# Kernel tuning notes

Measured on AMD Instinct MI355X. Metric: run time of the kernel, lower is better.

The kernel has to match this reference:

```python
import jax, jax.numpy as jnp
import numpy as np
from jax import lax

N_LAYERS = 10
N_BLOCKS = 3
N_STACK = N_LAYERS * N_BLOCKS  # 30
WIDTH = 512
SKIP_W = 256
CH = 1
QUANT = 256
BOTTLENECK = 16
KSIZE = 3
SCALE = 2 ** (N_LAYERS - 1)  # 512, nearest upsample factor
B, T = 1, 16384
T_EMB = T // SCALE  # 32


def causal_conv(x, w, b, dilation):
    # x: [B,Cin,T], w: [Cout,Cin,K] -> causal dilated conv, output [B,Cout,T]
    k = w.shape[-1]
    pad = (k - 1) * dilation
    y = lax.conv_general_dilated(x, w, window_strides=(1,), padding=[(pad, 0)],
                                 rhs_dilation=(dilation,),
                                 dimension_numbers=('NCH', 'OIH', 'NCH'))
    return y + b[None, :, None]


def conv1x1(x, w, b):
    # x: [B,Cin,T], w: [Cout,Cin]
    return jnp.einsum('oc,bct->bot', w, x) + b[None, :, None]


def setup_inputs() -> dict:
    key = jax.random.key(0)
    ks = jax.random.split(key, 24)
    s = 0.05
    inp = {
        'x': jax.random.normal(ks[0], (B, CH, T), jnp.float32),
        'embedding': jax.random.normal(ks[1], (B, BOTTLENECK, T_EMB), jnp.float32),
        'w_init': jax.random.normal(ks[2], (WIDTH, CH, KSIZE), jnp.float32) * s,
        'b_init': jnp.zeros((WIDTH,), jnp.float32),
        'w_iskip': jax.random.normal(ks[3], (SKIP_W, WIDTH), jnp.float32) * s,
        'b_iskip': jnp.zeros((SKIP_W,), jnp.float32),
        'w_dil': jax.random.normal(ks[4], (N_STACK, 2 * WIDTH, WIDTH, KSIZE), jnp.float32) * s,
        'b_dil': jnp.zeros((N_STACK, 2 * WIDTH), jnp.float32),
        'w_cond': jax.random.normal(ks[5], (N_STACK, 2 * WIDTH, BOTTLENECK), jnp.float32) * s,
        'b_cond': jnp.zeros((N_STACK, 2 * WIDTH), jnp.float32),
        'w_res': jax.random.normal(ks[6], (N_STACK, WIDTH, WIDTH), jnp.float32) * s,
        'b_res': jnp.zeros((N_STACK, WIDTH), jnp.float32),
        'w_skip': jax.random.normal(ks[7], (N_STACK, SKIP_W, WIDTH), jnp.float32) * s,
        'b_skip': jnp.zeros((N_STACK, SKIP_W), jnp.float32),
        'w_fskip': jax.random.normal(ks[8], (SKIP_W, SKIP_W), jnp.float32) * s,
        'b_fskip': jnp.zeros((SKIP_W,), jnp.float32),
        'w_fcond': jax.random.normal(ks[9], (SKIP_W, BOTTLENECK), jnp.float32) * s,
        'b_fcond': jnp.zeros((SKIP_W,), jnp.float32),
        'w_quant': jax.random.normal(ks[10], (QUANT, SKIP_W), jnp.float32) * s,
        'b_quant': jnp.zeros((QUANT,), jnp.float32),
    }
    return inp


def reference(x, embedding, w_init, b_init, w_iskip, b_iskip, w_dil, b_dil,
              w_cond, b_cond, w_res, b_res, w_skip, b_skip,
              w_fskip, b_fskip, w_fcond, b_fcond, w_quant, b_quant):
    # initial causal conv (kernel 3, dilation 1) + initial skip 1x1
    h = causal_conv(x, w_init, b_init, 1)            # [B,WIDTH,T]
    skip = conv1x1(h, w_iskip, b_iskip)              # [B,SKIP_W,T]
    for i in range(N_STACK):
        dilation = 2 ** (i % N_LAYERS)
        cond = conv1x1(embedding, w_cond[i], b_cond[i])      # [B,2W,T_EMB]
        cond_up = jnp.repeat(cond, SCALE, axis=-1)           # nearest upsample -> [B,2W,T]
        dilated = causal_conv(h, w_dil[i], b_dil[i], dilation) + cond_up
        filters = jax.nn.sigmoid(dilated[:, :WIDTH, :])
        gates = jnp.tanh(dilated[:, WIDTH:, :])
        pre = filters * gates
        h = h + conv1x1(pre, w_res[i], b_res[i])
        skip = skip + conv1x1(pre, w_skip[i], b_skip[i])
    skip = conv1x1(jax.nn.relu(skip), w_fskip, b_fskip)
    fcond = jnp.repeat(conv1x1(embedding, w_fcond, b_fcond), SCALE, axis=-1)
    skip = skip + fcond
    return conv1x1(jax.nn.relu(skip), w_quant, b_quant)     # [B,QUANT,T]
```

## Files before the change

kernel.cpp:

```cpp
#include <hip/hip_runtime.h>


typedef _Float16 f16x8 __attribute__((ext_vector_type(8)));
typedef float f32x4 __attribute__((ext_vector_type(4)));

#define NSTACK 30
#define TLEN   16384

typedef __attribute__((address_space(1))) const unsigned int glob_u32;
typedef __attribute__((address_space(3))) unsigned int lds_u32;

__device__ __forceinline__ void gll16(const unsigned short* g, unsigned short* l) {
  __builtin_amdgcn_global_load_lds((glob_u32*)g, (lds_u32*)l, 16, 0, 0);
}

__device__ __forceinline__ unsigned short f2h(float x) {
  union { _Float16 h; unsigned short u; } c;
  c.h = (_Float16)x;
  return c.u;
}
__device__ __forceinline__ unsigned pack2(float a, float b) {
  return (unsigned)f2h(a) | ((unsigned)f2h(b) << 16);
}
__device__ __forceinline__ float uplo(unsigned u){ union{unsigned v;_Float16 h[2];}c; c.v=u; return (float)c.h[0]; }
__device__ __forceinline__ float uphi(unsigned u){ union{unsigned v;_Float16 h[2];}c; c.v=u; return (float)c.h[1]; }
__device__ __forceinline__ f16x8 ldh(const unsigned short* p) {
  return *(const f16x8*)p;
}
__device__ __forceinline__ float sigmoidf_(float x){ return 1.0f/(1.0f+__expf(-x)); }
__device__ __forceinline__ float tanhf_(float x){ return 1.0f - 2.0f/(__expf(2.0f*x)+1.0f); }
#define MFMA16(a,b,c) __builtin_amdgcn_mfma_f32_16x16x32_f16((a),(b),(c),0,0,0)


__global__ void cast_f16_kernel(const float* __restrict__ src,
                                unsigned short* __restrict__ dst, int n4) {
  int g = blockIdx.x*256 + threadIdx.x;
  if (g >= n4) return;
  f32x4 v = *(const f32x4*)(src + 4*(size_t)g);
  unsigned int* d = (unsigned int*)(dst + 4*(size_t)g);
  d[0] = pack2(v[0], v[1]);
  d[1] = pack2(v[2], v[3]);
}

__global__ void transpose_wdil_kernel(const float* __restrict__ src,
                                      unsigned short* __restrict__ dst) {
  int g = blockIdx.x*256 + threadIdx.x;
  if (g >= NSTACK*1024*512) return;
  int c = g & 511;
  int m = (g >> 9) & 1023;
  int i = g >> 19;
  const float* s = src + (size_t)g*3;
  #pragma unroll
  for (int tap=0; tap<3; ++tap)
    dst[(((size_t)i*3+tap)*1024 + m)*512 + c] = f2h(s[tap]);
}

__global__ void cond_kernel(const float* __restrict__ emb,
                            const float* __restrict__ w_cond, const float* __restrict__ b_cond,
                            const float* __restrict__ b_dil,
                            const float* __restrict__ w_fcond, const float* __restrict__ b_fcond,
                            float* __restrict__ cond_all, float* __restrict__ fcond_all) {
  int g = blockIdx.x*256 + threadIdx.x;
  if (g < NSTACK*1024) {
    float acc[32];
    float base = b_cond[g] + b_dil[g];
    #pragma unroll
    for (int e=0;e<32;++e) acc[e] = base;
    #pragma unroll
    for (int c=0;c<16;++c) {
      float wv = w_cond[(size_t)g*16 + c];
      #pragma unroll
      for (int e=0;e<32;++e) acc[e] += wv * emb[c*32+e];
    }
    #pragma unroll
    for (int e=0;e<32;++e) cond_all[(size_t)g*32+e] = acc[e];
  } else if (g < NSTACK*1024 + 256) {
    int m = g - NSTACK*1024;
    float acc[32];
    float base = b_fcond[m];
    #pragma unroll
    for (int e=0;e<32;++e) acc[e] = base;
    #pragma unroll
    for (int c=0;c<16;++c) {
      float wv = w_fcond[(size_t)m*16 + c];
      #pragma unroll
      for (int e=0;e<32;++e) acc[e] += wv * emb[c*32+e];
    }
    #pragma unroll
    for (int e=0;e<32;++e) fcond_all[(size_t)m*32+e] = acc[e];
  }
}

__global__ void h0_kernel(const float* __restrict__ x, const float* __restrict__ w_init,
                          const float* __restrict__ b_init,
                          unsigned short* __restrict__ h_h16) {
  int g = blockIdx.x*256 + threadIdx.x;
  int t = g >> 7;
  int c = (g & 127) << 2;
  float xm2 = (t>=2)? x[t-2] : 0.f;
  float xm1 = (t>=1)? x[t-1] : 0.f;
  float x0  = x[t];
  float hv[4];
  #pragma unroll
  for (int r=0;r<4;++r) {
    int cc = c + r;
    hv[r] = w_init[cc*3+0]*xm2 + w_init[cc*3+1]*xm1 + w_init[cc*3+2]*x0 + b_init[cc];
  }
  unsigned int* hb = (unsigned int*)&h_h16[(size_t)t*512 + c];
  hb[0] = pack2(hv[0],hv[1]); hb[1] = pack2(hv[2],hv[3]);
}

__global__ __launch_bounds__(512) void skip_init_kernel(
    const unsigned short* __restrict__ h_h16, const unsigned short* __restrict__ Wiskip,
    const float* __restrict__ b_iskip, unsigned short* __restrict__ skip16) {
  int tid=threadIdx.x, w=tid>>6, l=tid&63, lr=l&15, lc=l>>4;
  int tb = blockIdx.x<<6;
  f32x4 acc[2][4];
  #pragma unroll
  for (int mf=0;mf<2;++mf)
    #pragma unroll
    for (int nf=0;nf<4;++nf) acc[mf][nf] = {0.f,0.f,0.f,0.f};
  for (int kc=0;kc<512;kc+=32) {
    f16x8 b[4];
    #pragma unroll
    for (int nf=0;nf<4;++nf)
      b[nf] = ldh(&h_h16[(size_t)(tb+16*nf+lr)*512 + kc + lc*8]);
    #pragma unroll
    for (int mf=0;mf<2;++mf) {
      f16x8 a = ldh(&Wiskip[(size_t)(w*32+16*mf+lr)*512 + kc + lc*8]);
      #pragma unroll
      for (int nf=0;nf<4;++nf)
        acc[mf][nf] = MFMA16(a, b[nf], acc[mf][nf]);
    }
  }
  #pragma unroll
  for (int mf=0;mf<2;++mf)
    #pragma unroll
    for (int nf=0;nf<4;++nf) {
      int s0 = w*32+16*mf+4*lc;
      int t  = tb+16*nf+lr;
      unsigned int* pp = (unsigned int*)&skip16[(size_t)t*256+s0];
      pp[0] = pack2(acc[mf][nf][0]+b_iskip[s0+0], acc[mf][nf][1]+b_iskip[s0+1]);
      pp[1] = pack2(acc[mf][nf][2]+b_iskip[s0+2], acc[mf][nf][3]+b_iskip[s0+3]);
    }
}

__global__ __launch_bounds__(256, 4) void dil_kernel(
    const unsigned short* __restrict__ h_in,
    unsigned short* __restrict__ pre,
    const unsigned short* __restrict__ A_dil,
    const float* __restrict__ cond,
    const unsigned short* __restrict__ zerobuf,
    int dilation) {
  __shared__ unsigned short Ab[2][128][32];
  __shared__ unsigned short Bb[2][128][32];
  const int tid = threadIdx.x;
  const int w = tid >> 6, l = tid & 63;
  const int lr = l & 15, lc = l >> 4;
  const int nt = blockIdx.x & 127, mt = blockIdx.x >> 7;
  const int tb = nt << 7;
  const int e  = tb >> 9;
  const int wr = w >> 1, wc = w & 1;

  const int srowA0 = (w<<5) + (l>>2);
  const int schunk = (l & 3) << 3;

  f32x4 fa[2][4], ga[2][4];
  #pragma unroll
  for (int mf=0;mf<2;++mf)
    #pragma unroll
    for (int nf=0;nf<4;++nf) { fa[mf][nf] = {0.f,0.f,0.f,0.f}; ga[mf][nf] = {0.f,0.f,0.f,0.f}; }

  auto stage = [&](int buf, int s){
    const int tap = s >> 4;
    const int kc  = (s & 15) << 5;
    const int shift = (2 - tap) * dilation;
    const unsigned short* Abase = A_dil + (size_t)tap * (1024*512) + kc + schunk;
    #pragma unroll
    for (int j=0;j<2;++j){
      const int r = srowA0 + (j<<4);
      const int m = mt*64 + r + ((r>>6)*448);
      gll16(Abase + (size_t)m*512, &Ab[buf][(w<<5)+(j<<4)][0]);
      const int t = tb + r - shift;
      const unsigned short* srcB = (t >= 0) ? (h_in + (size_t)t*512 + kc + schunk)
                                            : (zerobuf + schunk);
      gll16(srcB, &Bb[buf][(w<<5)+(j<<4)][0]);
    }
  };

  stage(0, 0);
  for (int s=0; s<48; ++s) {
    const int cur = s & 1;
    __syncthreads();
    if (s+1 < 48) stage(cur^1, s+1);
    f16x8 af[2], ag[2], bf[4];
    #pragma unroll
    for (int mf=0;mf<2;++mf){
      const int row = (wr<<5) + (mf<<4) + lr;
      af[mf] = ldh(&Ab[cur][row][lc<<3]);
      ag[mf] = ldh(&Ab[cur][64+row][lc<<3]);
    }
    #pragma unroll
    for (int nf=0;nf<4;++nf)
      bf[nf] = ldh(&Bb[cur][(wc<<6)+(nf<<4)+lr][lc<<3]);
    #pragma unroll
    for (int mf=0;mf<2;++mf)
      #pragma unroll
      for (int nf=0;nf<4;++nf){
        fa[mf][nf] = MFMA16(af[mf], bf[nf], fa[mf][nf]);
        ga[mf][nf] = MFMA16(ag[mf], bf[nf], ga[mf][nf]);
      }
  }

  #pragma unroll
  for (int mf=0;mf<2;++mf)
    #pragma unroll
    for (int nf=0;nf<4;++nf){
      const int m0 = mt*64 + (wr<<5) + (mf<<4) + (lc<<2);
      const int t  = tb + (wc<<6) + (nf<<4) + lr;
      float pv[4];
      #pragma unroll
      for (int r=0;r<4;++r){
        float f = fa[mf][nf][r] + cond[(size_t)(m0+r)*32 + e];
        float g = ga[mf][nf][r] + cond[(size_t)(m0+r+512)*32 + e];
        pv[r] = sigmoidf_(f) * tanhf_(g);
      }
      unsigned int* pp = (unsigned int*)&pre[(size_t)t*512 + m0];
      pp[0] = pack2(pv[0], pv[1]);
      pp[1] = pack2(pv[2], pv[3]);
    }
}

__global__ __launch_bounds__(256, 3) void ressk_kernel(
    const unsigned short* __restrict__ pre,
    const unsigned short* __restrict__ h_in,
    unsigned short* __restrict__ h_out,
    unsigned short* __restrict__ skip16,
    const unsigned short* __restrict__ Wres,
    const unsigned short* __restrict__ Wskip,
    const float* __restrict__ b_res,
    const float* __restrict__ b_skip) {
  __shared__ unsigned short Ab[2][128][32];
  __shared__ unsigned short Bb[2][128][32];
  const int tid = threadIdx.x;
  const int w = tid >> 6, l = tid & 63;
  const int lr = l & 15, lc = l >> 4;
  const int nt = blockIdx.x & 127, mt = blockIdx.x >> 7;
  const int tb = nt << 7;
  const int wr = w >> 1, wc = w & 1;
  const bool isres = (mt < 4);
  const unsigned short* W = isres ? Wres : Wskip;
  const int mrow0 = (isres ? mt : (mt-4)) * 128;

  const int srowA0 = (w<<5) + (l>>2);
  const int schunk = (l & 3) << 3;

  f32x4 acc[4][4];
  #pragma unroll
  for (int mf=0;mf<4;++mf)
    #pragma unroll
    for (int nf=0;nf<4;++nf) acc[mf][nf] = {0.f,0.f,0.f,0.f};

  auto stage = [&](int buf, int s){
    const int kc = s << 5;
    #pragma unroll
    for (int j=0;j<2;++j){
      const int r = srowA0 + (j<<4);
      gll16(W + (size_t)(mrow0 + r)*512 + kc + schunk, &Ab[buf][(w<<5)+(j<<4)][0]);
      gll16(pre + (size_t)(tb + r)*512 + kc + schunk, &Bb[buf][(w<<5)+(j<<4)][0]);
    }
  };

  stage(0, 0);
  for (int s=0; s<16; ++s) {
    const int cur = s & 1;
    __syncthreads();
    if (s+1 < 16) stage(cur^1, s+1);
    f16x8 a[4], bf[4];
    #pragma unroll
    for (int mf=0;mf<4;++mf)
      a[mf] = ldh(&Ab[cur][(wr<<6)+(mf<<4)+lr][lc<<3]);
    #pragma unroll
    for (int nf=0;nf<4;++nf)
      bf[nf] = ldh(&Bb[cur][(wc<<6)+(nf<<4)+lr][lc<<3]);
    #pragma unroll
    for (int mf=0;mf<4;++mf)
      #pragma unroll
      for (int nf=0;nf<4;++nf)
        acc[mf][nf] = MFMA16(a[mf], bf[nf], acc[mf][nf]);
  }

  if (isres) {
    #pragma unroll
    for (int mf=0;mf<4;++mf)
      #pragma unroll
      for (int nf=0;nf<4;++nf){
        const int m0 = mrow0 + (wr<<6) + (mf<<4) + (lc<<2);
        const int t  = tb + (wc<<6) + (nf<<4) + lr;
        const unsigned int* hi = (const unsigned int*)&h_in[(size_t)t*512 + m0];
        unsigned int h01 = hi[0], h23 = hi[1];
        float v0 = uplo(h01) + acc[mf][nf][0] + b_res[m0+0];
        float v1 = uphi(h01) + acc[mf][nf][1] + b_res[m0+1];
        float v2 = uplo(h23) + acc[mf][nf][2] + b_res[m0+2];
        float v3 = uphi(h23) + acc[mf][nf][3] + b_res[m0+3];
        unsigned int* hb = (unsigned int*)&h_out[(size_t)t*512 + m0];
        hb[0] = pack2(v0,v1); hb[1] = pack2(v2,v3);
      }
  } else {
    #pragma unroll
    for (int mf=0;mf<4;++mf)
      #pragma unroll
      for (int nf=0;nf<4;++nf){
        const int s0 = mrow0 + (wr<<6) + (mf<<4) + (lc<<2);
        const int t  = tb + (wc<<6) + (nf<<4) + lr;
        unsigned int* sp = (unsigned int*)&skip16[(size_t)t*256 + s0];
        unsigned int s01 = sp[0], s23 = sp[1];
        float v0 = uplo(s01) + acc[mf][nf][0] + b_skip[s0+0];
        float v1 = uphi(s01) + acc[mf][nf][1] + b_skip[s0+1];
        float v2 = uplo(s23) + acc[mf][nf][2] + b_skip[s0+2];
        float v3 = uphi(s23) + acc[mf][nf][3] + b_skip[s0+3];
        sp[0] = pack2(v0,v1); sp[1] = pack2(v2,v3);
      }
  }
}

__global__ __launch_bounds__(512) void final_kernel(
    const unsigned short* __restrict__ skip16, const unsigned short* __restrict__ Wfs,
    const float* __restrict__ b_fskip, const float* __restrict__ fcond,
    const unsigned short* __restrict__ Wq, const float* __restrict__ b_quant,
    float* __restrict__ out) {
  __shared__ unsigned short S1[64][264];
  __shared__ unsigned short S2[64][264];
  int tid=threadIdx.x, w=tid>>6, l=tid&63, lr=l&15, lc=l>>4;
  int tb = blockIdx.x<<6, e = tb>>9;

  for (int j = tid; j < 64*32; j += 512) {
    int r  = j >> 5;
    int c8 = (j & 31) << 3;
    const unsigned int* sp = (const unsigned int*)&skip16[(size_t)(tb+r)*256 + c8];
    unsigned int* dp = (unsigned int*)&S1[r][c8];
    #pragma unroll
    for (int q=0;q<4;++q){
      unsigned int u = sp[q];
      dp[q] = pack2(fmaxf(uplo(u),0.f), fmaxf(uphi(u),0.f));
    }
  }
  __syncthreads();

  f32x4 acc[2][4];
  #pragma unroll
  for (int mf=0;mf<2;++mf)
    #pragma unroll
    for (int nf=0;nf<4;++nf) acc[mf][nf] = {0.f,0.f,0.f,0.f};
  for (int kc=0;kc<256;kc+=32) {
    f16x8 b[4];
    #pragma unroll
    for (int nf=0;nf<4;++nf) b[nf] = ldh(&S1[16*nf+lr][kc + lc*8]);
    #pragma unroll
    for (int mf=0;mf<2;++mf) {
      f16x8 a = ldh(&Wfs[(size_t)(w*32+16*mf+lr)*256 + kc + lc*8]);
      #pragma unroll
      for (int nf=0;nf<4;++nf)
        acc[mf][nf] = MFMA16(a, b[nf], acc[mf][nf]);
    }
  }
  #pragma unroll
  for (int mf=0;mf<2;++mf)
    #pragma unroll
    for (int nf=0;nf<4;++nf) {
      int m0 = w*32+16*mf+4*lc;
      int n  = 16*nf+lr;
      float pv[4];
      #pragma unroll
      for (int r=0;r<4;++r) {
        float v = acc[mf][nf][r] + b_fskip[m0+r] + fcond[(size_t)(m0+r)*32 + e];
        pv[r] = fmaxf(v, 0.f);
      }
      unsigned int* pp = (unsigned int*)&S2[n][m0];
      pp[0] = pack2(pv[0],pv[1]); pp[1] = pack2(pv[2],pv[3]);
    }
  __syncthreads();

  f32x4 acc2[2][4];
  #pragma unroll
  for (int mf=0;mf<2;++mf)
    #pragma unroll
    for (int nf=0;nf<4;++nf) acc2[mf][nf] = {0.f,0.f,0.f,0.f};
  for (int kc=0;kc<256;kc+=32) {
    f16x8 b[4];
    #pragma unroll
    for (int nf=0;nf<4;++nf) b[nf] = ldh(&S2[16*nf+lr][kc + lc*8]);
    #pragma unroll
    for (int mf=0;mf<2;++mf) {
      f16x8 a = ldh(&Wq[(size_t)(w*32+16*mf+lr)*256 + kc + lc*8]);
      #pragma unroll
      for (int nf=0;nf<4;++nf)
        acc2[mf][nf] = MFMA16(a, b[nf], acc2[mf][nf]);
    }
  }
  #pragma unroll
  for (int mf=0;mf<2;++mf)
    #pragma unroll
    for (int nf=0;nf<4;++nf) {
      int q0 = w*32+16*mf+4*lc;
      int t  = tb + 16*nf + lr;
      #pragma unroll
      for (int r=0;r<4;++r)
        out[(size_t)(q0+r)*TLEN + t] = acc2[mf][nf][r] + b_quant[q0+r];
    }
}


extern "C" void kernel_launch(void* const* d_in, const int* in_sizes, int n_in,
                              void* d_out, int out_size, void* d_ws, size_t ws_size,
                              hipStream_t stream) {
  const float* x       = (const float*)d_in[0];
  const float* emb     = (const float*)d_in[1];
  const float* w_init  = (const float*)d_in[2];
  const float* b_init  = (const float*)d_in[3];
  const float* w_iskip = (const float*)d_in[4];
  const float* b_iskip = (const float*)d_in[5];
  const float* w_dil   = (const float*)d_in[6];
  const float* b_dil   = (const float*)d_in[7];
  const float* w_cond  = (const float*)d_in[8];
  const float* b_cond  = (const float*)d_in[9];
  const float* w_res   = (const float*)d_in[10];
  const float* b_res   = (const float*)d_in[11];
  const float* w_skip  = (const float*)d_in[12];
  const float* b_skip  = (const float*)d_in[13];
  const float* w_fskip = (const float*)d_in[14];
  const float* b_fskip = (const float*)d_in[15];
  const float* w_fcond = (const float*)d_in[16];
  const float* b_fcond = (const float*)d_in[17];
  const float* w_quant = (const float*)d_in[18];
  const float* b_quant = (const float*)d_in[19];
  float* out = (float*)d_out;

  char* ws = (char*)d_ws;
  size_t off = 0;
  auto carve = [&](size_t bytes) -> void* {
    void* p = ws + off;
    off += (bytes + 255) & ~(size_t)255;
    return p;
  };
  unsigned short* A_dil     = (unsigned short*)carve((size_t)NSTACK*3*1024*512*2);
  unsigned short* Wres_h    = (unsigned short*)carve((size_t)NSTACK*512*512*2);
  unsigned short* Wskip_h   = (unsigned short*)carve((size_t)NSTACK*256*512*2);
  unsigned short* Wiskip_h  = (unsigned short*)carve((size_t)256*512*2);
  unsigned short* Wfskip_h  = (unsigned short*)carve((size_t)256*256*2);
  unsigned short* Wquant_h  = (unsigned short*)carve((size_t)256*256*2);
  unsigned short* h_h16     = (unsigned short*)carve((size_t)2*TLEN*512*2);
  unsigned short* pre_h16   = (unsigned short*)carve((size_t)TLEN*512*2);
  unsigned short* skip_h16  = (unsigned short*)carve((size_t)TLEN*256*2);
  float*          cond_all  = (float*)carve((size_t)NSTACK*1024*32*4);
  float*          fcond_all = (float*)carve((size_t)256*32*4);
  unsigned short* zerobuf   = (unsigned short*)carve((size_t)512*2);
  if (off > ws_size) return;

  hipMemsetAsync(zerobuf, 0, 512*2, stream);

  cast_f16_kernel<<<(NSTACK*512*512/4 + 255)/256, 256, 0, stream>>>(w_res,   Wres_h,   NSTACK*512*512/4);
  cast_f16_kernel<<<(NSTACK*256*512/4 + 255)/256, 256, 0, stream>>>(w_skip,  Wskip_h,  NSTACK*256*512/4);
  cast_f16_kernel<<<(256*512/4 + 255)/256,        256, 0, stream>>>(w_iskip, Wiskip_h, 256*512/4);
  cast_f16_kernel<<<(256*256/4 + 255)/256,        256, 0, stream>>>(w_fskip, Wfskip_h, 256*256/4);
  cast_f16_kernel<<<(256*256/4 + 255)/256,        256, 0, stream>>>(w_quant, Wquant_h, 256*256/4);
  transpose_wdil_kernel<<<(NSTACK*1024*512 + 255)/256, 256, 0, stream>>>(w_dil, A_dil);
  cond_kernel<<<(NSTACK*1024 + 256 + 255)/256, 256, 0, stream>>>(
      emb, w_cond, b_cond, b_dil, w_fcond, b_fcond, cond_all, fcond_all);

  h0_kernel<<<TLEN*128/256, 256, 0, stream>>>(x, w_init, b_init, h_h16);
  skip_init_kernel<<<TLEN/64, 512, 0, stream>>>(h_h16, Wiskip_h, b_iskip, skip_h16);

  const size_t HB = (size_t)TLEN*512;
  for (int i = 0; i < NSTACK; ++i) {
    int d = 1 << (i % 10);
    const unsigned short* h_in = h_h16 + (size_t)(i & 1)*HB;
    unsigned short* h_out      = h_h16 + (size_t)((i + 1) & 1)*HB;
    dil_kernel<<<1024, 256, 0, stream>>>(
        h_in,
        pre_h16,
        A_dil + (size_t)i*3*1024*512,
        cond_all + (size_t)i*1024*32,
        zerobuf,
        d);
    ressk_kernel<<<768, 256, 0, stream>>>(
        pre_h16,
        h_in,
        h_out,
        skip_h16,
        Wres_h + (size_t)i*512*512,
        Wskip_h + (size_t)i*256*512,
        b_res + (size_t)i*512,
        b_skip + (size_t)i*256);
  }

  final_kernel<<<TLEN/64, 512, 0, stream>>>(
      skip_h16, Wfskip_h, b_fskip, fcond_all, Wquant_h, b_quant, out);
}
```

Before: 3.114 ms.

## Fuse dilated-conv and residual/skip kernels per layer with per-tile flag sync

Merges the per-layer dilated gated conv kernel and the res/skip 1x1 kernel into one launch of 1792 blocks. The res/skip blocks spin on per-time-tile atomic counters until all 8 producer blocks for their tile have written pre. This lets res/skip work on finished tiles overlap with the remaining dilated conv work and removes one launch per layer. It relies on blocks being dispatched in index order to avoid deadlock, and spinning blocks hold CU slots while they wait.

```diff
diff --git a/kernel.cpp b/kernel.cpp
--- a/kernel.cpp
+++ b/kernel.cpp
@@ -30,6 +30,14 @@
 __device__ __forceinline__ float sigmoidf_(float x){ return 1.0f/(1.0f+__expf(-x)); }
 __device__ __forceinline__ float tanhf_(float x){ return 1.0f - 2.0f/(__expf(2.0f*x)+1.0f); }
 #define MFMA16(a,b,c) __builtin_amdgcn_mfma_f32_16x16x32_f16((a),(b),(c),0,0,0)
+
+__device__ __forceinline__ void spin_ge(int* p, int v){
+  while (__hip_atomic_load(p, __ATOMIC_ACQUIRE, __HIP_MEMORY_SCOPE_AGENT) < v)
+    __builtin_amdgcn_s_sleep(2);
+}
+__device__ __forceinline__ void flag_add(int* p){
+  __hip_atomic_fetch_add(p, 1, __ATOMIC_RELEASE, __HIP_MEMORY_SCOPE_AGENT);
+}
 
 
 __global__ void cast_f16_kernel(const float* __restrict__ src,
@@ -145,115 +153,112 @@
     }
 }
 
-__global__ __launch_bounds__(256, 4) void dil_kernel(
+__global__ __launch_bounds__(256, 4) void layer_kernel(
     const unsigned short* __restrict__ h_in,
+    unsigned short* __restrict__ h_out,
     unsigned short* __restrict__ pre,
+    unsigned short* __restrict__ skip16,
     const unsigned short* __restrict__ A_dil,
+    const unsigned short* __restrict__ Wres,
+    const unsigned short* __restrict__ Wskip,
     const float* __restrict__ cond,
+    const float* __restrict__ b_res,
+    const float* __restrict__ b_skip,
     const unsigned short* __restrict__ zerobuf,
-    int dilation) {
+    int dilation,
+    int* __restrict__ pre_cnt) {
   __shared__ unsigned short Ab[2][128][32];
   __shared__ unsigned short Bb[2][128][32];
   const int tid = threadIdx.x;
   const int w = tid >> 6, l = tid & 63;
   const int lr = l & 15, lc = l >> 4;
-  const int nt = blockIdx.x & 127, mt = blockIdx.x >> 7;
-  const int tb = nt << 7;
-  const int e  = tb >> 9;
   const int wr = w >> 1, wc = w & 1;
-
   const int srowA0 = (w<<5) + (l>>2);
   const int schunk = (l & 3) << 3;
 
-  f32x4 fa[2][4], ga[2][4];
-  #pragma unroll
-  for (int mf=0;mf<2;++mf)
-    #pragma unroll
-    for (int nf=0;nf<4;++nf) { fa[mf][nf] = {0.f,0.f,0.f,0.f}; ga[mf][nf] = {0.f,0.f,0.f,0.f}; }
-
-  auto stage = [&](int buf, int s){
-    const int tap = s >> 4;
-    const int kc  = (s & 15) << 5;
-    const int shift = (2 - tap) * dilation;
-    const unsigned short* Abase = A_dil + (size_t)tap * (1024*512) + kc + schunk;
-    #pragma unroll
-    for (int j=0;j<2;++j){
-      const int r = srowA0 + (j<<4);
-      const int m = mt*64 + r + ((r>>6)*448);
-      gll16(Abase + (size_t)m*512, &Ab[buf][(w<<5)+(j<<4)][0]);
-      const int t = tb + r - shift;
-      const unsigned short* srcB = (t >= 0) ? (h_in + (size_t)t*512 + kc + schunk)
-                                            : (zerobuf + schunk);
-      gll16(srcB, &Bb[buf][(w<<5)+(j<<4)][0]);
-    }
-  };
-
-  stage(0, 0);
-  for (int s=0; s<48; ++s) {
-    const int cur = s & 1;
+  if (blockIdx.x < 1024) {
+    const int nt = blockIdx.x & 127, mt = blockIdx.x >> 7;
+    const int tb = nt << 7;
+    const int e  = tb >> 9;
+
+    f32x4 fa[2][4], ga[2][4];
+    #pragma unroll
+    for (int mf=0;mf<2;++mf)
+      #pragma unroll
+      for (int nf=0;nf<4;++nf) { fa[mf][nf] = {0.f,0.f,0.f,0.f}; ga[mf][nf] = {0.f,0.f,0.f,0.f}; }
+
+    auto stage = [&](int buf, int s){
+      const int tap = s >> 4;
+      const int kc  = (s & 15) << 5;
+      const int shift = (2 - tap) * dilation;
+      const unsigned short* Abase = A_dil + (size_t)tap * (1024*512) + kc + schunk;
+      #pragma unroll
+      for (int j=0;j<2;++j){
+        const int r = srowA0 + (j<<4);
+        const int m = mt*64 + r + ((r>>6)*448);
+        gll16(Abase + (size_t)m*512, &Ab[buf][(w<<5)+(j<<4)][0]);
+        const int t = tb + r - shift;
+        const unsigned short* srcB = (t >= 0) ? (h_in + (size_t)t*512 + kc + schunk)
+                                              : (zerobuf + schunk);
+        gll16(srcB, &Bb[buf][(w<<5)+(j<<4)][0]);
+      }
+    };
+
+    stage(0, 0);
+    for (int s=0; s<48; ++s) {
+      const int cur = s & 1;
+      __syncthreads();
+      if (s+1 < 48) stage(cur^1, s+1);
+      f16x8 af[2], ag[2], bf[4];
+      #pragma unroll
+      for (int mf=0;mf<2;++mf){
+        const int row = (wr<<5) + (mf<<4) + lr;
+        af[mf] = ldh(&Ab[cur][row][lc<<3]);
+        ag[mf] = ldh(&Ab[cur][64+row][lc<<3]);
+      }
+      #pragma unroll
+      for (int nf=0;nf<4;++nf)
+        bf[nf] = ldh(&Bb[cur][(wc<<6)+(nf<<4)+lr][lc<<3]);
+      #pragma unroll
+      for (int mf=0;mf<2;++mf)
+        #pragma unroll
+        for (int nf=0;nf<4;++nf){
+          fa[mf][nf] = MFMA16(af[mf], bf[nf], fa[mf][nf]);
+          ga[mf][nf] = MFMA16(ag[mf], bf[nf], ga[mf][nf]);
+        }
+    }
+
+    #pragma unroll
+    for (int mf=0;mf<2;++mf)
+      #pragma unroll
+      for (int nf=0;nf<4;++nf){
+        const int m0 = mt*64 + (wr<<5) + (mf<<4) + (lc<<2);
+        const int t  = tb + (wc<<6) + (nf<<4) + lr;
+        float pv[4];
+        #pragma unroll
+        for (int r=0;r<4;++r){
+          float f = fa[mf][nf][r] + cond[(size_t)(m0+r)*32 + e];
+          float g = ga[mf][nf][r] + cond[(size_t)(m0+r+512)*32 + e];
+          pv[r] = sigmoidf_(f) * tanhf_(g);
+        }
+        unsigned int* pp = (unsigned int*)&pre[(size_t)t*512 + m0];
+        pp[0] = pack2(pv[0], pv[1]);
+        pp[1] = pack2(pv[2], pv[3]);
+      }
     __syncthreads();
-    if (s+1 < 48) stage(cur^1, s+1);
-    f16x8 af[2], ag[2], bf[4];
-    #pragma unroll
-    for (int mf=0;mf<2;++mf){
-      const int row = (wr<<5) + (mf<<4) + lr;
-      af[mf] = ldh(&Ab[cur][row][lc<<3]);
-      ag[mf] = ldh(&Ab[cur][64+row][lc<<3]);
-    }
-    #pragma unroll
-    for (int nf=0;nf<4;++nf)
-      bf[nf] = ldh(&Bb[cur][(wc<<6)+(nf<<4)+lr][lc<<3]);
-    #pragma unroll
-    for (int mf=0;mf<2;++mf)
-      #pragma unroll
-      for (int nf=0;nf<4;++nf){
-        fa[mf][nf] = MFMA16(af[mf], bf[nf], fa[mf][nf]);
-        ga[mf][nf] = MFMA16(ag[mf], bf[nf], ga[mf][nf]);
-      }
-  }
-
-  #pragma unroll
-  for (int mf=0;mf<2;++mf)
-    #pragma unroll
-    for (int nf=0;nf<4;++nf){
-      const int m0 = mt*64 + (wr<<5) + (mf<<4) + (lc<<2);
-      const int t  = tb + (wc<<6) + (nf<<4) + lr;
-      float pv[4];
-      #pragma unroll
-      for (int r=0;r<4;++r){
-        float f = fa[mf][nf][r] + cond[(size_t)(m0+r)*32 + e];
-        float g = ga[mf][nf][r] + cond[(size_t)(m0+r+512)*32 + e];
-        pv[r] = sigmoidf_(f) * tanhf_(g);
-      }
-      unsigned int* pp = (unsigned int*)&pre[(size_t)t*512 + m0];
-      pp[0] = pack2(pv[0], pv[1]);
-      pp[1] = pack2(pv[2], pv[3]);
-    }
-}
-
-__global__ __launch_bounds__(256, 3) void ressk_kernel(
-    const unsigned short* __restrict__ pre,
-    const unsigned short* __restrict__ h_in,
-    unsigned short* __restrict__ h_out,
-    unsigned short* __restrict__ skip16,
-    const unsigned short* __restrict__ Wres,
-    const unsigned short* __restrict__ Wskip,
-    const float* __restrict__ b_res,
-    const float* __restrict__ b_skip) {
-  __shared__ unsigned short Ab[2][128][32];
-  __shared__ unsigned short Bb[2][128][32];
-  const int tid = threadIdx.x;
-  const int w = tid >> 6, l = tid & 63;
-  const int lr = l & 15, lc = l >> 4;
-  const int nt = blockIdx.x & 127, mt = blockIdx.x >> 7;
+    if (tid == 0){ __threadfence(); flag_add(&pre_cnt[nt]); }
+    return;
+  }
+
+  const int b2 = blockIdx.x - 1024;
+  const int nt = b2 & 127, rk = b2 >> 7;
   const int tb = nt << 7;
-  const int wr = w >> 1, wc = w & 1;
-  const bool isres = (mt < 4);
+  const bool isres = (rk < 4);
   const unsigned short* W = isres ? Wres : Wskip;
-  const int mrow0 = (isres ? mt : (mt-4)) * 128;
-
-  const int srowA0 = (w<<5) + (l>>2);
-  const int schunk = (l & 3) << 3;
+  const int mrow0 = (isres ? rk : (rk-4)) * 128;
+
+  if (tid == 0) spin_ge(&pre_cnt[nt], 8);
+  __syncthreads();
 
   f32x4 acc[4][4];
   #pragma unroll
@@ -261,7 +266,7 @@
     #pragma unroll
     for (int nf=0;nf<4;++nf) acc[mf][nf] = {0.f,0.f,0.f,0.f};
 
-  auto stage = [&](int buf, int s){
+  auto stage2 = [&](int buf, int s){
     const int kc = s << 5;
     #pragma unroll
     for (int j=0;j<2;++j){
@@ -271,11 +276,11 @@
     }
   };
 
-  stage(0, 0);
+  stage2(0, 0);
   for (int s=0; s<16; ++s) {
     const int cur = s & 1;
     __syncthreads();
-    if (s+1 < 16) stage(cur^1, s+1);
+    if (s+1 < 16) stage2(cur^1, s+1);
     f16x8 a[4], bf[4];
     #pragma unroll
     for (int mf=0;mf<4;++mf)
@@ -455,9 +460,11 @@
   float*          cond_all  = (float*)carve((size_t)NSTACK*1024*32*4);
   float*          fcond_all = (float*)carve((size_t)256*32*4);
   unsigned short* zerobuf   = (unsigned short*)carve((size_t)512*2);
+  int*            flags     = (int*)carve((size_t)NSTACK*128*4);
   if (off > ws_size) return;
 
   hipMemsetAsync(zerobuf, 0, 512*2, stream);
+  hipMemsetAsync(flags, 0, (size_t)NSTACK*128*4, stream);
 
   cast_f16_kernel<<<(NSTACK*512*512/4 + 255)/256, 256, 0, stream>>>(w_res,   Wres_h,   NSTACK*512*512/4);
   cast_f16_kernel<<<(NSTACK*256*512/4 + 255)/256, 256, 0, stream>>>(w_skip,  Wskip_h,  NSTACK*256*512/4);
@@ -476,22 +483,20 @@
     int d = 1 << (i % 10);
     const unsigned short* h_in = h_h16 + (size_t)(i & 1)*HB;
     unsigned short* h_out      = h_h16 + (size_t)((i + 1) & 1)*HB;
-    dil_kernel<<<1024, 256, 0, stream>>>(
-        h_in,
-        pre_h16,
-        A_dil + (size_t)i*3*1024*512,
-        cond_all + (size_t)i*1024*32,
-        zerobuf,
-        d);
-    ressk_kernel<<<768, 256, 0, stream>>>(
-        pre_h16,
+    layer_kernel<<<1792, 256, 0, stream>>>(
         h_in,
         h_out,
+        pre_h16,
         skip_h16,
+        A_dil + (size_t)i*3*1024*512,
         Wres_h + (size_t)i*512*512,
         Wskip_h + (size_t)i*256*512,
+        cond_all + (size_t)i*1024*32,
         b_res + (size_t)i*512,
-        b_skip + (size_t)i*256);
+        b_skip + (size_t)i*256,
+        zerobuf,
+        d,
+        flags + (size_t)i*128);
   }
 
   final_kernel<<<TLEN/64, 512, 0, stream>>>(
```

Result: slower. 6.376 ms (+104.8%).
